# Performance work log

Hardware: AMD Instinct MI355X
Metric: run time of the kernel (lower is better)

Reference implementation:

```python
import jax, jax.numpy as jnp
import numpy as np

B, T, C, H = 4, 2048, 1024, 16
D = C // H


def setup_inputs() -> dict:
    key = jax.random.key(0)
    ks = jax.random.split(key, 5)
    s = 0.02
    return {
        "x": jax.random.normal(ks[0], (B, T, C), dtype=jnp.float32),
        "W_attn": jax.random.normal(ks[1], (C, 3 * C), dtype=jnp.float32) * s,
        "b_attn": jax.random.normal(ks[2], (3 * C,), dtype=jnp.float32) * s,
        "W_proj": jax.random.normal(ks[3], (C, C), dtype=jnp.float32) * s,
        "b_proj": jax.random.normal(ks[4], (C,), dtype=jnp.float32) * s,
    }


def reference(x, W_attn, b_attn, W_proj, b_proj):
    # QKV projection: [B,T,3C]
    qkv = x @ W_attn + b_attn
    q, k, v = jnp.split(qkv, 3, axis=-1)
    # [B,T,C] -> [B,H,T,D]
    def to_heads(t):
        return t.reshape(B, T, H, D).transpose(0, 2, 1, 3)
    q, k, v = to_heads(q), to_heads(k), to_heads(v)
    scale = 1.0 / np.sqrt(D).astype(np.float32)
    # full (non-causal) attention scores [B,H,T,T]
    att = jnp.einsum("bhqd,bhkd->bhqk", q, k) * scale
    att = jax.nn.softmax(att, axis=-1)
    y = jnp.einsum("bhqk,bhkd->bhqd", att, v)
    y = y.transpose(0, 2, 1, 3).reshape(B, T, C)
    return y @ W_proj + b_proj
```

## Files before the change

### kernel.cpp

```cpp
#include <hip/hip_runtime.h>

#define BATCH 4
#define SEQ   2048
#define CDIM  1024
#define NHEAD 16
#define HDIM  64
#define BH    (BATCH * NHEAD)
#define MROWS (BATCH * SEQ)

typedef __attribute__((ext_vector_type(8))) short  short8;
typedef __attribute__((ext_vector_type(4))) float  floatx4;

#define MFMA_BF16(a, b, c) __builtin_amdgcn_mfma_f32_16x16x32_bf16((a), (b), (c), 0, 0, 0)

#define GLOAD16(g, l) __builtin_amdgcn_global_load_lds( \
    (__attribute__((address_space(1))) void*)(g),       \
    (__attribute__((address_space(3))) void*)(l), 16, 0, 0)

__device__ __forceinline__ unsigned short f2bf(float f) {
    union { float f; unsigned u; } v; v.f = f;
    unsigned u = v.u;
    return (unsigned short)((u + 0x7FFFu + ((u >> 16) & 1u)) >> 16);
}

__device__ __forceinline__ float fast_exp2(float x) {
#if __has_builtin(__builtin_amdgcn_exp2f)
    return __builtin_amdgcn_exp2f(x);
#else
    return exp2f(x);
#endif
}

__device__ __forceinline__ unsigned pack_bf16_trunc(float a, float b) {
    union { float f; unsigned u; } ua, ub;
    ua.f = a; ub.f = b;
    return __builtin_amdgcn_perm(ub.u, ua.u, 0x07060302u);
}

__global__ __launch_bounds__(256) void conv_bf16_kernel(
    const float* __restrict__ in, unsigned short* __restrict__ out)
{
    int i = (blockIdx.x * 256 + threadIdx.x) * 4;
    float4 v = *(const float4*)(in + i);
    ushort4 o;
    o.x = f2bf(v.x); o.y = f2bf(v.y); o.z = f2bf(v.z); o.w = f2bf(v.w);
    *(ushort4*)(out + i) = o;
}

__global__ __launch_bounds__(256) void conv_wt_kernel(
    const float* __restrict__ in, unsigned short* __restrict__ out, int K, int N)
{
    __shared__ float T[64][68];
    const int k0 = blockIdx.y * 64, n0 = blockIdx.x * 64;
    const int tid = threadIdx.x;
    const int r = tid >> 4, c4 = (tid & 15) * 4;
    #pragma unroll
    for (int i = 0; i < 4; ++i) {
        int row = r + i * 16;
        float4 v = *(const float4*)(in + (size_t)(k0 + row) * N + n0 + c4);
        T[row][c4 + 0] = v.x; T[row][c4 + 1] = v.y;
        T[row][c4 + 2] = v.z; T[row][c4 + 3] = v.w;
    }
    __syncthreads();
    #pragma unroll
    for (int i = 0; i < 4; ++i) {
        int nrow = r + i * 16;
        ushort4 o;
        o.x = f2bf(T[c4 + 0][nrow]); o.y = f2bf(T[c4 + 1][nrow]);
        o.z = f2bf(T[c4 + 2][nrow]); o.w = f2bf(T[c4 + 3][nrow]);
        *(ushort4*)(out + (size_t)(n0 + nrow) * K + k0 + c4) = o;
    }
}

__global__ __launch_bounds__(512, 2) void qkv_mfma_kernel(
    const unsigned short* __restrict__ A,
    const unsigned short* __restrict__ Bt,
    const float* __restrict__ bias,
    unsigned short* __restrict__ Qo,
    unsigned short* __restrict__ Ko,
    unsigned short* __restrict__ Vo)
{
    __shared__ __align__(16) unsigned short L[2 * 32768];

    const int tid = threadIdx.x;
    const int m0 = blockIdx.y * 256, n0 = blockIdx.x * 256;
    const int w = tid >> 6, lane = tid & 63;
    const int wr = w >> 2, wc = w & 3;
    const int lm = lane & 15, kg = lane >> 4;
    const int sw = lm & 7;

    floatx4 acc[2][4][2][2];
    const floatx4 zf = {0.f, 0.f, 0.f, 0.f};
    #pragma unroll
    for (int a = 0; a < 2; ++a)
        #pragma unroll
        for (int b = 0; b < 4; ++b)
            #pragma unroll
            for (int c = 0; c < 2; ++c)
                #pragma unroll
                for (int d = 0; d < 2; ++d) acc[a][b][c][d] = zf;

    short8 af[4][2], bf[2][2];

#define QSTAGE_A(B_, H_, KT_) do {                                            \
    unsigned short* _l = (unsigned short*)L + (B_) * 32768 + (H_) * 8192;     \
    _Pragma("unroll")                                                         \
    for (int _i = 0; _i < 2; ++_i) {                                          \
        int _s = _i * 512 + tid, _r = _s >> 3, _c = _s & 7;                   \
        GLOAD16(A + (size_t)(m0 + (H_) * 128 + _r) * CDIM + (KT_) * 64        \
                   + ((_c ^ (_r & 7)) * 8), _l + _s * 8);                     \
    } } while (0)

#define QSTAGE_B(B_, H_, KT_) do {                                            \
    unsigned short* _l = (unsigned short*)L + (B_) * 32768 + 16384 + (H_) * 8192; \
    _Pragma("unroll")                                                         \
    for (int _i = 0; _i < 2; ++_i) {                                          \
        int _s = _i * 512 + tid, _r = _s >> 3, _c = _s & 7;                   \
        GLOAD16(Bt + (size_t)(n0 + (H_) * 128 + _r) * CDIM + (KT_) * 64       \
                   + ((_c ^ (_r & 7)) * 8), _l + _s * 8);                     \
    } } while (0)

#define QLOAD_A(B_, H_) do {                                                  \
    const unsigned short* _p = (const unsigned short*)L + (B_) * 32768 + (H_) * 8192; \
    _Pragma("unroll")                                                         \
    for (int _m = 0; _m < 4; ++_m) {                                          \
        int _row = wr * 64 + _m * 16 + lm;                                    \
        _Pragma("unroll")                                                     \
        for (int _k = 0; _k < 2; ++_k)                                        \
            af[_m][_k] = *(const short8*)(_p + _row * 64                      \
                          + (((_k * 4 + kg) ^ sw) * 8));                      \
    } } while (0)

#define QLOAD_B(B_, H_) do {                                                  \
    const unsigned short* _p = (const unsigned short*)L + (B_) * 32768 + 16384 + (H_) * 8192; \
    _Pragma("unroll")                                                         \
    for (int _n = 0; _n < 2; ++_n) {                                          \
        int _row = wc * 32 + _n * 16 + lm;                                    \
        _Pragma("unroll")                                                     \
        for (int _k = 0; _k < 2; ++_k)                                        \
            bf[_n][_k] = *(const short8*)(_p + _row * 64                      \
                          + (((_k * 4 + kg) ^ sw) * 8));                      \
    } } while (0)

#define QMFMA(HH_, HP_) do {                                                  \
    _Pragma("unroll") for (int _k = 0; _k < 2; ++_k)                          \
    _Pragma("unroll") for (int _m = 0; _m < 4; ++_m)                          \
    _Pragma("unroll") for (int _n = 0; _n < 2; ++_n)                          \
        acc[HH_][_m][HP_][_n] =                                               \
            MFMA_BF16(af[_m][_k], bf[_n][_k], acc[HH_][_m][HP_][_n]);         \
    } while (0)

#define QPHASE(HH_, HP_, LA_, LB_, STAGE_, VM_) do {                          \
    if (LA_) QLOAD_A(buf, HH_);                                               \
    if (LB_) QLOAD_B(buf, HP_);                                               \
    STAGE_;                                                                   \
    asm volatile("s_waitcnt vmcnt(" #VM_ ")" ::: "memory");                   \
    __builtin_amdgcn_s_barrier();                                             \
    asm volatile("s_waitcnt lgkmcnt(0)" ::: "memory");                        \
    __builtin_amdgcn_sched_barrier(0);                                        \
    __builtin_amdgcn_s_setprio(1);                                            \
    QMFMA(HH_, HP_);                                                          \
    __builtin_amdgcn_s_setprio(0);                                            \
    __builtin_amdgcn_s_barrier();                                             \
    __builtin_amdgcn_sched_barrier(0);                                        \
    } while (0)

    QSTAGE_A(0, 0, 0); QSTAGE_B(0, 0, 0); QSTAGE_B(0, 1, 0); QSTAGE_A(0, 1, 0);
    asm volatile("s_waitcnt vmcnt(4)" ::: "memory");
    __builtin_amdgcn_s_barrier();

    #pragma unroll 1
    for (int t = 0; t < CDIM / 64 - 1; ++t) {
        const int buf = t & 1, nb = buf ^ 1;
        QPHASE(0, 0, 1, 1, QSTAGE_A(nb, 0, t + 1), 4);
        QPHASE(0, 1, 0, 1, QSTAGE_B(nb, 0, t + 1), 4);
        QPHASE(1, 1, 1, 0, QSTAGE_B(nb, 1, t + 1), 4);
        QPHASE(1, 0, 0, 1, QSTAGE_A(nb, 1, t + 1), 4);
    }
    {
        const int buf = (CDIM / 64 - 1) & 1;
        QPHASE(0, 0, 1, 1, ((void)0), 2);
        QPHASE(0, 1, 0, 1, ((void)0), 0);
        QPHASE(1, 1, 1, 0, ((void)0), 0);
        QPHASE(1, 0, 0, 1, ((void)0), 0);
    }

#undef QPHASE
#undef QMFMA
#undef QLOAD_B
#undef QLOAD_A
#undef QSTAGE_B
#undef QSTAGE_A

    #pragma unroll
    for (int hp = 0; hp < 2; ++hp) {
        #pragma unroll
        for (int nt = 0; nt < 2; ++nt) {
            int col = n0 + hp * 128 + wc * 32 + nt * 16 + lm;
            float bv = bias[col];
            int which = col >> 10;
            int c1 = col & 1023;
            int h = c1 >> 6, d = c1 & 63;
            #pragma unroll
            for (int hh = 0; hh < 2; ++hh) {
                #pragma unroll
                for (int mt = 0; mt < 4; ++mt) {
                    int m = m0 + hh * 128 + wr * 64 + mt * 16 + kg * 4;
                    int b = m >> 11;
                    int tt = m & 2047;
                    int bh = b * NHEAD + h;
                    floatx4 a = acc[hh][mt][hp][nt];
                    if (which == 2) {
                        ushort4 o;
                        o.x = f2bf(a[0] + bv);
                        o.y = f2bf(a[1] + bv);
                        o.z = f2bf(a[2] + bv);
                        o.w = f2bf(a[3] + bv);
                        *(ushort4*)(Vo + ((size_t)bh * 64 + d) * SEQ + tt) = o;
                    } else {
                        unsigned short* dst = (which == 0) ? Qo : Ko;
                        float qs = (which == 0) ? 0.18033688011112042f : 1.0f;
                        #pragma unroll
                        for (int r = 0; r < 4; ++r)
                            dst[((size_t)bh * SEQ + tt + r) * 64 + d] =
                                f2bf((a[r] + bv) * qs);
                    }
                }
            }
        }
    }
}

#define GBUF (128 * 32)

__device__ __forceinline__ void gemm_stage(
    const unsigned short* __restrict__ A, const unsigned short* __restrict__ Bt,
    int K, int m0, int n0, int k0, unsigned short* As, unsigned short* Bs, int tid)
{
    #pragma unroll
    for (int i = 0; i < 2; ++i) {
        int ci = i * 256 + tid;
        GLOAD16(A  + (size_t)(m0 + (ci >> 2)) * K + k0 + (ci & 3) * 8, As + ci * 8);
        GLOAD16(Bt + (size_t)(n0 + (ci >> 2)) * K + k0 + (ci & 3) * 8, Bs + ci * 8);
    }
}

__global__ __launch_bounds__(256) void proj_mfma_kernel(
    const unsigned short* __restrict__ A,
    const unsigned short* __restrict__ Bt,
    const float* __restrict__ bias,
    float* __restrict__ out)
{
    const int K = CDIM;
    __shared__ __align__(16) unsigned short As2[2 * GBUF];
    __shared__ __align__(16) unsigned short Bs2[2 * GBUF];

    const int tid = threadIdx.x;
    const int m0 = blockIdx.y * 128, n0 = blockIdx.x * 128;
    const int w = tid >> 6, lane = tid & 63;
    const int wm = (w >> 1) * 64, wn = (w & 1) * 64;
    const int lm = lane & 15, kg = lane >> 4;

    floatx4 acc[4][4];
    const floatx4 zf = {0.f, 0.f, 0.f, 0.f};
    #pragma unroll
    for (int mt = 0; mt < 4; ++mt)
        #pragma unroll
        for (int nt = 0; nt < 4; ++nt) acc[mt][nt] = zf;

    gemm_stage(A, Bt, K, m0, n0, 0, As2, Bs2, tid);

    #pragma unroll 1
    for (int kt = 0; kt < K / 32; ++kt) {
        __syncthreads();
        if (kt + 1 < K / 32)
            gemm_stage(A, Bt, K, m0, n0, (kt + 1) * 32,
                       As2 + ((kt + 1) & 1) * GBUF, Bs2 + ((kt + 1) & 1) * GBUF, tid);
        const unsigned short* As = As2 + (kt & 1) * GBUF;
        const unsigned short* Bs = Bs2 + (kt & 1) * GBUF;
        short8 af[4], bfr[4];
        #pragma unroll
        for (int t = 0; t < 4; ++t) {
            af[t]  = *(const short8*)(As + (wm + t * 16 + lm) * 32 + kg * 8);
            bfr[t] = *(const short8*)(Bs + (wn + t * 16 + lm) * 32 + kg * 8);
        }
        #pragma unroll
        for (int mt = 0; mt < 4; ++mt)
            #pragma unroll
            for (int nt = 0; nt < 4; ++nt)
                acc[mt][nt] = MFMA_BF16(af[mt], bfr[nt], acc[mt][nt]);
    }

    #pragma unroll
    for (int nt = 0; nt < 4; ++nt) {
        int col = n0 + wn + nt * 16 + lm;
        float bv = bias[col];
        #pragma unroll
        for (int mt = 0; mt < 4; ++mt) {
            int mbase = m0 + wm + mt * 16 + kg * 4;
            #pragma unroll
            for (int r = 0; r < 4; ++r)
                out[(size_t)(mbase + r) * CDIM + col] = acc[mt][nt][r] + bv;
        }
    }
}

#define BUFSH 8192

__device__ __forceinline__ void attn_stage_tile(
    const unsigned short* __restrict__ Kg,
    const unsigned short* __restrict__ Vg,
    size_t base, int kb, unsigned short* buf, int tid)
{
    unsigned short* Kb_ = buf;
    unsigned short* Vb_ = buf + 4096;
    #pragma unroll
    for (int i = 0; i < 2; ++i) {
        int lin = i * 256 + tid;
        int srow = lin >> 3;
        int chunk = lin & 7;
        int s2 = srow & 31;
        int grow = (srow & 32) + ((s2 >> 2) & 3) * 8 + ((s2 >> 4) & 1) * 4 + (s2 & 3);
        int gch = chunk ^ (srow & 7);
        GLOAD16(Kg + base + (size_t)(kb * 64 + grow) * 64 + gch * 8, Kb_ + lin * 8);
        GLOAD16(Vg + base + (size_t)srow * SEQ + kb * 64 + gch * 8, Vb_ + lin * 8);
    }
}

__global__ __launch_bounds__(256) void attn_mfma_kernel(
    const unsigned short* __restrict__ Qg,
    const unsigned short* __restrict__ Kg,
    const unsigned short* __restrict__ Vg,
    unsigned short* __restrict__ Y)
{
    __shared__ __align__(16) unsigned short Smem[2 * BUFSH];

    const int tid = threadIdx.x, w = tid >> 6, lane = tid & 63;
    const int lm = lane & 15, kg = lane >> 4;
    const int qb = blockIdx.x, bh = blockIdx.y;
    const size_t base = (size_t)bh * SEQ * 64;

    short8 qf[4][2];
    #pragma unroll
    for (int nt = 0; nt < 4; ++nt)
        #pragma unroll
        for (int c = 0; c < 2; ++c)
            qf[nt][c] = *(const short8*)(
                Qg + base + (size_t)(qb * 256 + w * 64 + nt * 16 + lm) * 64 + c * 32 + kg * 8);

    const floatx4 zf = {0.f, 0.f, 0.f, 0.f};
    floatx4 O[4][4];
    #pragma unroll
    for (int nt = 0; nt < 4; ++nt)
        #pragma unroll
        for (int nd = 0; nd < 4; ++nd) O[nt][nd] = zf;
    float lsum[4] = {0.f, 0.f, 0.f, 0.f};

    attn_stage_tile(Kg, Vg, base, 0, Smem, tid);

    #pragma unroll 1
    for (int kb = 0; kb < SEQ / 64; ++kb) {
        __syncthreads();
        if (kb + 1 < SEQ / 64)
            attn_stage_tile(Kg, Vg, base, kb + 1, Smem + ((kb + 1) & 1) * BUFSH, tid);

        const unsigned short* Ksb = Smem + (kb & 1) * BUFSH;
        const unsigned short* Vsb = Ksb + 4096;
        const int sw = (lm & 7);

        #pragma unroll
        for (int ch = 0; ch < 2; ++ch) {
            uint4 pa[4];
            #pragma unroll
            for (int mt = 0; mt < 2; ++mt) {
                floatx4 st[4];
                #pragma unroll
                for (int nt = 0; nt < 4; ++nt) st[nt] = zf;
                #pragma unroll
                for (int c = 0; c < 2; ++c) {
                    short8 kf = *(const short8*)(
                        Ksb + (ch * 32 + mt * 16 + lm) * 64 + ((c * 4 + kg) ^ sw) * 8);
                    #pragma unroll
                    for (int nt = 0; nt < 4; ++nt)
                        st[nt] = MFMA_BF16(kf, qf[nt][c], st[nt]);
                }
                #pragma unroll
                for (int nt = 0; nt < 4; ++nt) {
                    float e0 = fast_exp2(st[nt][0]);
                    float e1 = fast_exp2(st[nt][1]);
                    float e2 = fast_exp2(st[nt][2]);
                    float e3 = fast_exp2(st[nt][3]);
                    lsum[nt] += (e0 + e1) + (e2 + e3);
                    if (mt == 0) {
                        pa[nt].x = pack_bf16_trunc(e0, e1);
                        pa[nt].y = pack_bf16_trunc(e2, e3);
                    } else {
                        pa[nt].z = pack_bf16_trunc(e0, e1);
                        pa[nt].w = pack_bf16_trunc(e2, e3);
                    }
                }
            }
            #pragma unroll
            for (int nd = 0; nd < 4; ++nd) {
                short8 vb = *(const short8*)(
                    Vsb + (nd * 16 + lm) * 64 + ((ch * 4 + kg) ^ sw) * 8);
                #pragma unroll
                for (int nt = 0; nt < 4; ++nt) {
                    short8 paf;
                    __builtin_memcpy(&paf, &pa[nt], 16);
                    O[nt][nd] = MFMA_BF16(paf, vb, O[nt][nd]);
                }
            }
        }
    }

    #pragma unroll
    for (int nt = 0; nt < 4; ++nt) {
        lsum[nt] += __shfl_xor(lsum[nt], 16);
        lsum[nt] += __shfl_xor(lsum[nt], 32);
    }
    float linv[4][4];
    #pragma unroll
    for (int mq = 0; mq < 4; ++mq)
        #pragma unroll
        for (int r = 0; r < 4; ++r)
            linv[mq][r] = 1.0f / __shfl(lsum[mq], kg * 4 + r);

    const int b = bh >> 4, h = bh & 15;
    #pragma unroll
    for (int mq = 0; mq < 4; ++mq)
        #pragma unroll
        for (int r = 0; r < 4; ++r) {
            int t = qb * 256 + w * 64 + mq * 16 + kg * 4 + r;
            #pragma unroll
            for (int nd = 0; nd < 4; ++nd)
                Y[((size_t)(b * SEQ + t)) * CDIM + h * 64 + nd * 16 + lm] =
                    f2bf(O[mq][nd][r] * linv[mq][r]);
        }
}

extern "C" void kernel_launch(void* const* d_in, const int* in_sizes, int n_in,
                              void* d_out, int out_size, void* d_ws, size_t ws_size,
                              hipStream_t stream) {
    const float* x      = (const float*)d_in[0];
    const float* W_attn = (const float*)d_in[1];
    const float* b_attn = (const float*)d_in[2];
    const float* W_proj = (const float*)d_in[3];
    const float* b_proj = (const float*)d_in[4];
    float* out = (float*)d_out;

    char* ws = (char*)d_ws;
    unsigned short* xb  = (unsigned short*)(ws);
    unsigned short* Wat = (unsigned short*)(ws + (size_t)16777216);
    unsigned short* Wpt = (unsigned short*)(ws + (size_t)23068672);
    unsigned short* Qb  = (unsigned short*)(ws + (size_t)25165824);
    unsigned short* Kb  = (unsigned short*)(ws + (size_t)41943040);
    unsigned short* Vtb = (unsigned short*)(ws + (size_t)58720256);
    unsigned short* Yb  = (unsigned short*)(ws + (size_t)75497472);

    conv_bf16_kernel<<<dim3(MROWS * CDIM / 1024), 256, 0, stream>>>(x, xb);
    conv_wt_kernel<<<dim3(3 * CDIM / 64, CDIM / 64), 256, 0, stream>>>(
        W_attn, Wat, CDIM, 3 * CDIM);
    conv_wt_kernel<<<dim3(CDIM / 64, CDIM / 64), 256, 0, stream>>>(
        W_proj, Wpt, CDIM, CDIM);

    qkv_mfma_kernel<<<dim3(3 * CDIM / 256, MROWS / 256), 512, 0, stream>>>(
        xb, Wat, b_attn, Qb, Kb, Vtb);

    attn_mfma_kernel<<<dim3(SEQ / 256, BH), 256, 0, stream>>>(Qb, Kb, Vtb, Yb);

    proj_mfma_kernel<<<dim3(CDIM / 128, MROWS / 128), 256, 0, stream>>>(
        Yb, Wpt, b_proj, out);
}
```

Before: 269.7 us.

## Rewrite output projection GEMM with 256x256 tiles and phased pipelining

Rewrites the output-projection GEMM to use 256x256 block tiles, 512 threads and a K-step of 64. Global-to-LDS loads use an XOR-swizzled layout to reduce bank conflicts. Each K-step is split into four quadrant phases that interleave prefetch of the next tile with MFMA work, using explicit waitcnt, barriers and setprio. The goal is more data reuse per LDS load and better overlap of memory with compute, at the cost of a larger LDS footprint (128KB), more registers and only 128 blocks in the grid.

```diff
diff --git a/kernel.cpp b/kernel.cpp
--- a/kernel.cpp
+++ b/kernel.cpp
@@ -231,76 +231,141 @@
     }
 }
 
-#define GBUF (128 * 32)
-
-__device__ __forceinline__ void gemm_stage(
-    const unsigned short* __restrict__ A, const unsigned short* __restrict__ Bt,
-    int K, int m0, int n0, int k0, unsigned short* As, unsigned short* Bs, int tid)
-{
-    #pragma unroll
-    for (int i = 0; i < 2; ++i) {
-        int ci = i * 256 + tid;
-        GLOAD16(A  + (size_t)(m0 + (ci >> 2)) * K + k0 + (ci & 3) * 8, As + ci * 8);
-        GLOAD16(Bt + (size_t)(n0 + (ci >> 2)) * K + k0 + (ci & 3) * 8, Bs + ci * 8);
-    }
-}
-
-__global__ __launch_bounds__(256) void proj_mfma_kernel(
+__global__ __launch_bounds__(512, 2) void proj_mfma_kernel(
     const unsigned short* __restrict__ A,
     const unsigned short* __restrict__ Bt,
     const float* __restrict__ bias,
     float* __restrict__ out)
 {
-    const int K = CDIM;
-    __shared__ __align__(16) unsigned short As2[2 * GBUF];
-    __shared__ __align__(16) unsigned short Bs2[2 * GBUF];
+    __shared__ __align__(16) unsigned short L[2 * 32768];
 
     const int tid = threadIdx.x;
-    const int m0 = blockIdx.y * 128, n0 = blockIdx.x * 128;
+    const int m0 = blockIdx.y * 256, n0 = blockIdx.x * 256;
     const int w = tid >> 6, lane = tid & 63;
-    const int wm = (w >> 1) * 64, wn = (w & 1) * 64;
+    const int wr = w >> 2, wc = w & 3;
     const int lm = lane & 15, kg = lane >> 4;
-
-    floatx4 acc[4][4];
+    const int sw = lm & 7;
+
+    floatx4 acc[2][4][2][2];
     const floatx4 zf = {0.f, 0.f, 0.f, 0.f};
     #pragma unroll
-    for (int mt = 0; mt < 4; ++mt)
-        #pragma unroll
-        for (int nt = 0; nt < 4; ++nt) acc[mt][nt] = zf;
-
-    gemm_stage(A, Bt, K, m0, n0, 0, As2, Bs2, tid);
+    for (int a = 0; a < 2; ++a)
+        #pragma unroll
+        for (int b = 0; b < 4; ++b)
+            #pragma unroll
+            for (int c = 0; c < 2; ++c)
+                #pragma unroll
+                for (int d = 0; d < 2; ++d) acc[a][b][c][d] = zf;
+
+    short8 af[4][2], bf[2][2];
+
+#define PSTAGE_A(B_, H_, KT_) do {                                            \
+    unsigned short* _l = (unsigned short*)L + (B_) * 32768 + (H_) * 8192;     \
+    _Pragma("unroll")                                                         \
+    for (int _i = 0; _i < 2; ++_i) {                                          \
+        int _s = _i * 512 + tid, _r = _s >> 3, _c = _s & 7;                   \
+        GLOAD16(A + (size_t)(m0 + (H_) * 128 + _r) * CDIM + (KT_) * 64        \
+                   + ((_c ^ (_r & 7)) * 8), _l + _s * 8);                     \
+    } } while (0)
+
+#define PSTAGE_B(B_, H_, KT_) do {                                            \
+    unsigned short* _l = (unsigned short*)L + (B_) * 32768 + 16384 + (H_) * 8192; \
+    _Pragma("unroll")                                                         \
+    for (int _i = 0; _i < 2; ++_i) {                                          \
+        int _s = _i * 512 + tid, _r = _s >> 3, _c = _s & 7;                   \
+        GLOAD16(Bt + (size_t)(n0 + (H_) * 128 + _r) * CDIM + (KT_) * 64       \
+                   + ((_c ^ (_r & 7)) * 8), _l + _s * 8);                     \
+    } } while (0)
+
+#define PLOAD_A(B_, H_) do {                                                  \
+    const unsigned short* _p = (const unsigned short*)L + (B_) * 32768 + (H_) * 8192; \
+    _Pragma("unroll")                                                         \
+    for (int _m = 0; _m < 4; ++_m) {                                          \
+        int _row = wr * 64 + _m * 16 + lm;                                    \
+        _Pragma("unroll")                                                     \
+        for (int _k = 0; _k < 2; ++_k)                                        \
+            af[_m][_k] = *(const short8*)(_p + _row * 64                      \
+                          + (((_k * 4 + kg) ^ sw) * 8));                      \
+    } } while (0)
+
+#define PLOAD_B(B_, H_) do {                                                  \
+    const unsigned short* _p = (const unsigned short*)L + (B_) * 32768 + 16384 + (H_) * 8192; \
+    _Pragma("unroll")                                                         \
+    for (int _n = 0; _n < 2; ++_n) {                                          \
+        int _row = wc * 32 + _n * 16 + lm;                                    \
+        _Pragma("unroll")                                                     \
+        for (int _k = 0; _k < 2; ++_k)                                        \
+            bf[_n][_k] = *(const short8*)(_p + _row * 64                      \
+                          + (((_k * 4 + kg) ^ sw) * 8));                      \
+    } } while (0)
+
+#define PMFMA(HH_, HP_) do {                                                  \
+    _Pragma("unroll") for (int _k = 0; _k < 2; ++_k)                          \
+    _Pragma("unroll") for (int _m = 0; _m < 4; ++_m)                          \
+    _Pragma("unroll") for (int _n = 0; _n < 2; ++_n)                          \
+        acc[HH_][_m][HP_][_n] =                                               \
+            MFMA_BF16(af[_m][_k], bf[_n][_k], acc[HH_][_m][HP_][_n]);         \
+    } while (0)
+
+#define PPHASE(HH_, HP_, LA_, LB_, STAGE_, VM_) do {                          \
+    if (LA_) PLOAD_A(buf, HH_);                                               \
+    if (LB_) PLOAD_B(buf, HP_);                                               \
+    STAGE_;                                                                   \
+    asm volatile("s_waitcnt vmcnt(" #VM_ ")" ::: "memory");                   \
+    __builtin_amdgcn_s_barrier();                                             \
+    asm volatile("s_waitcnt lgkmcnt(0)" ::: "memory");                        \
+    __builtin_amdgcn_sched_barrier(0);                                        \
+    __builtin_amdgcn_s_setprio(1);                                            \
+    PMFMA(HH_, HP_);                                                          \
+    __builtin_amdgcn_s_setprio(0);                                            \
+    __builtin_amdgcn_s_barrier();                                             \
+    __builtin_amdgcn_sched_barrier(0);                                        \
+    } while (0)
+
+    PSTAGE_A(0, 0, 0); PSTAGE_B(0, 0, 0); PSTAGE_B(0, 1, 0); PSTAGE_A(0, 1, 0);
+    asm volatile("s_waitcnt vmcnt(4)" ::: "memory");
+    __builtin_amdgcn_s_barrier();
 
     #pragma unroll 1
-    for (int kt = 0; kt < K / 32; ++kt) {
-        __syncthreads();
-        if (kt + 1 < K / 32)
-            gemm_stage(A, Bt, K, m0, n0, (kt + 1) * 32,
-                       As2 + ((kt + 1) & 1) * GBUF, Bs2 + ((kt + 1) & 1) * GBUF, tid);
-        const unsigned short* As = As2 + (kt & 1) * GBUF;
-        const unsigned short* Bs = Bs2 + (kt & 1) * GBUF;
-        short8 af[4], bfr[4];
-        #pragma unroll
-        for (int t = 0; t < 4; ++t) {
-            af[t]  = *(const short8*)(As + (wm + t * 16 + lm) * 32 + kg * 8);
-            bfr[t] = *(const short8*)(Bs + (wn + t * 16 + lm) * 32 + kg * 8);
-        }
-        #pragma unroll
-        for (int mt = 0; mt < 4; ++mt)
-            #pragma unroll
-            for (int nt = 0; nt < 4; ++nt)
-                acc[mt][nt] = MFMA_BF16(af[mt], bfr[nt], acc[mt][nt]);
-    }
-
-    #pragma unroll
-    for (int nt = 0; nt < 4; ++nt) {
-        int col = n0 + wn + nt * 16 + lm;
-        float bv = bias[col];
-        #pragma unroll
-        for (int mt = 0; mt < 4; ++mt) {
-            int mbase = m0 + wm + mt * 16 + kg * 4;
-            #pragma unroll
-            for (int r = 0; r < 4; ++r)
-                out[(size_t)(mbase + r) * CDIM + col] = acc[mt][nt][r] + bv;
+    for (int t = 0; t < CDIM / 64 - 1; ++t) {
+        const int buf = t & 1, nb = buf ^ 1;
+        PPHASE(0, 0, 1, 1, PSTAGE_A(nb, 0, t + 1), 4);
+        PPHASE(0, 1, 0, 1, PSTAGE_B(nb, 0, t + 1), 4);
+        PPHASE(1, 1, 1, 0, PSTAGE_B(nb, 1, t + 1), 4);
+        PPHASE(1, 0, 0, 1, PSTAGE_A(nb, 1, t + 1), 4);
+    }
+    {
+        const int buf = (CDIM / 64 - 1) & 1;
+        PPHASE(0, 0, 1, 1, ((void)0), 2);
+        PPHASE(0, 1, 0, 1, ((void)0), 0);
+        PPHASE(1, 1, 1, 0, ((void)0), 0);
+        PPHASE(1, 0, 0, 1, ((void)0), 0);
+    }
+
+#undef PPHASE
+#undef PMFMA
+#undef PLOAD_B
+#undef PLOAD_A
+#undef PSTAGE_B
+#undef PSTAGE_A
+
+    #pragma unroll
+    for (int hp = 0; hp < 2; ++hp) {
+        #pragma unroll
+        for (int nt = 0; nt < 2; ++nt) {
+            int col = n0 + hp * 128 + wc * 32 + nt * 16 + lm;
+            float bv = bias[col];
+            #pragma unroll
+            for (int hh = 0; hh < 2; ++hh) {
+                #pragma unroll
+                for (int mt = 0; mt < 4; ++mt) {
+                    int row = m0 + hh * 128 + wr * 64 + mt * 16 + kg * 4;
+                    floatx4 a = acc[hh][mt][hp][nt];
+                    #pragma unroll
+                    for (int r = 0; r < 4; ++r)
+                        out[(size_t)(row + r) * CDIM + col] = a[r] + bv;
+                }
+            }
         }
     }
 }
@@ -469,6 +534,6 @@
 
     attn_mfma_kernel<<<dim3(SEQ / 256, BH), 256, 0, stream>>>(Qb, Kb, Vtb, Yb);
 
-    proj_mfma_kernel<<<dim3(CDIM / 128, MROWS / 128), 256, 0, stream>>>(
+    proj_mfma_kernel<<<dim3(CDIM / 256, MROWS / 256), 512, 0, stream>>>(
         Yb, Wpt, b_proj, out);
 }
```

After: 275.1 us. About the same (+2.0%).
